# Performance work log

Measured on AMD Instinct MI355X. Metric: run time of the kernel, lower is better.

## Reference

```python
import jax, jax.numpy as jnp
import numpy as np

N = 16384       # pedestrian_num
D_IN = 2        # input_size
H = 64          # hidden_size


def setup_inputs() -> dict:
    key = jax.random.key(0)
    ks = jax.random.split(key, 4)
    data = jax.random.normal(ks[0], (N, D_IN), dtype=jnp.float32)
    # Linear weights stored as [in, out]; scaled like torch default init (~1/sqrt(in)).
    W1 = jax.random.normal(ks[1], (D_IN, 32), dtype=jnp.float32) / np.sqrt(D_IN)
    b1 = jnp.zeros((32,), dtype=jnp.float32)
    W2 = jax.random.normal(ks[2], (32, 64), dtype=jnp.float32) / np.sqrt(32)
    b2 = jnp.zeros((64,), dtype=jnp.float32)
    W3 = jax.random.normal(ks[3], (64, H), dtype=jnp.float32) / np.sqrt(64)
    b3 = jnp.zeros((H,), dtype=jnp.float32)
    return {"data": data, "W1": W1, "b1": b1, "W2": W2, "b2": b2, "W3": W3, "b3": b3}


def reference(data, W1, b1, W2, b2, W3, b3):
    # Per-pedestrian MLP (batched over all N pedestrians at once).
    h = jax.nn.relu(data @ W1 + b1)          # [N, 32]
    h = jax.nn.relu(h @ W2 + b2)             # [N, 64]
    h = h @ W3 + b3                          # [N, H]
    # Spatial affinity: the original fills the lower triangle with <h_i, h_j>
    # and its softmax reads entry [max(i,j), min(i,j)], i.e. the full
    # symmetric Gram matrix G = h @ h.T.
    G = jnp.einsum("nd,md->nm", h, h)        # [N, N], symmetric
    # Row-wise softmax over the symmetric affinity matrix.
    return jax.nn.softmax(G, axis=-1)
```

## Files before the change

kernel.cpp:

```cpp
#include <hip/hip_runtime.h>

#define N     16384
#define DH    64
#define TILE  128
#define NT    (N / TILE)
#define S2    133

typedef __attribute__((ext_vector_type(8))) short  short8;
typedef __attribute__((ext_vector_type(4))) float  f32x4;

__device__ __forceinline__ ushort bf_hi(float x) {
    unsigned u = __float_as_uint(x);
    unsigned r = u + 0x7FFFu + ((u >> 16) & 1u);
    return (ushort)(r >> 16);
}
__device__ __forceinline__ float bf_val(ushort h) {
    return __uint_as_float(((unsigned)h) << 16);
}

__device__ __forceinline__ short8 ldfrag(const ushort* __restrict__ p, int row, int koff) {
    return *(const short8*)(p + (size_t)row * DH + koff);
}

__global__ __launch_bounds__(128) void mlp_kernel(
    const float* __restrict__ data,
    const float* __restrict__ W1, const float* __restrict__ b1,
    const float* __restrict__ W2, const float* __restrict__ b2,
    const float* __restrict__ W3, const float* __restrict__ b3,
    ushort* __restrict__ hHi, ushort* __restrict__ hLo)
{
    __shared__ float sW1[64], sb1[32], sW2[32 * 64], sb2[64], sW3[64 * 64], sb3[64];
    const int tid = threadIdx.x;
    if (tid < 64) sW1[tid] = W1[tid];
    if (tid < 32) sb1[tid] = b1[tid];
    if (tid < 64) sb2[tid] = b2[tid];
    if (tid < 64) sb3[tid] = b3[tid];
    for (int t = tid; t < 32 * 64; t += 128) sW2[t] = W2[t];
    for (int t = tid; t < 64 * 64; t += 128) sW3[t] = W3[t];
    __syncthreads();

    const int i = blockIdx.x * 128 + tid;
    const float x0 = data[2 * i + 0];
    const float x1 = data[2 * i + 1];

    float h1[32];
#pragma unroll
    for (int o = 0; o < 32; ++o)
        h1[o] = fmaxf(0.f, fmaf(x0, sW1[o], fmaf(x1, sW1[32 + o], sb1[o])));

    float h2[64];
#pragma unroll
    for (int o = 0; o < 64; ++o) {
        float a = sb2[o];
#pragma unroll
        for (int k = 0; k < 32; ++k) a = fmaf(h1[k], sW2[k * 64 + o], a);
        h2[o] = fmaxf(0.f, a);
    }

    ushort hs[64], ls[64];
#pragma unroll
    for (int o = 0; o < 64; ++o) {
        float a = sb3[o];
#pragma unroll
        for (int k = 0; k < 64; ++k) a = fmaf(h2[k], sW3[k * 64 + o], a);
        const ushort hb = bf_hi(a);
        hs[o] = hb;
        ls[o] = bf_hi(a - bf_val(hb));
    }
#pragma unroll
    for (int q = 0; q < 8; ++q) {
        short8 vh, vl;
#pragma unroll
        for (int t = 0; t < 8; ++t) { vh[t] = (short)hs[q * 8 + t]; vl[t] = (short)ls[q * 8 + t]; }
        *(short8*)(hHi + (size_t)i * DH + q * 8) = vh;
        *(short8*)(hLo + (size_t)i * DH + q * 8) = vl;
    }
}

__device__ __forceinline__ void stage_B(
    const ushort* __restrict__ hHi, const ushort* __restrict__ hLo,
    int brow0, int tid, ushort* __restrict__ sB)
{
    const int arr = tid >> 7;
    const int r   = tid & 127;
    const ushort* __restrict__ src = (arr ? hLo : hHi) + (size_t)(brow0 + r) * DH;
    ushort* __restrict__ dst = sB + arr * (TILE * DH) + r * 64;
    const int sw = (r & 7);
#pragma unroll
    for (int q = 0; q < 8; ++q) {
        const short8 v = *(const short8*)(src + q * 8);
        *(short8*)(dst + 8 * (q ^ sw)) = v;
    }
}

__device__ __forceinline__ short8 ldB(const ushort* __restrict__ sB,
                                      int arr, int row, int ks, int kb)
{
    return *(const short8*)(sB + arr * (TILE * DH) + row * 64 + 8 * (((ks << 2) + kb) ^ (row & 7)));
}

__device__ __forceinline__ void gram_tile(
    const ushort* __restrict__ hHi, const ushort* __restrict__ hLo,
    const ushort* __restrict__ sB,
    int bi, int wave, int r16, int kb, f32x4 acc[2][8])
{
#pragma unroll
    for (int rb = 0; rb < 2; ++rb)
#pragma unroll
        for (int cb = 0; cb < 8; ++cb) acc[rb][cb] = (f32x4){0.f, 0.f, 0.f, 0.f};

    const int arow = bi * TILE + wave * 16 + r16;
#pragma unroll
    for (int ks = 0; ks < 2; ++ks) {
        const int koff = ks * 32 + kb * 8;
        const short8 Ah0 = ldfrag(hHi, arow,      koff);
        const short8 Ah1 = ldfrag(hHi, arow + 64, koff);
        const short8 Al0 = ldfrag(hLo, arow,      koff);
        const short8 Al1 = ldfrag(hLo, arow + 64, koff);
#pragma unroll
        for (int cb = 0; cb < 8; ++cb) {
            const int brow = cb * 16 + r16;
            const short8 Bh = ldB(sB, 0, brow, ks, kb);
            const short8 Bl = ldB(sB, 1, brow, ks, kb);
            acc[0][cb] = __builtin_amdgcn_mfma_f32_16x16x32_bf16(Ah0, Bh, acc[0][cb], 0, 0, 0);
            acc[0][cb] = __builtin_amdgcn_mfma_f32_16x16x32_bf16(Ah0, Bl, acc[0][cb], 0, 0, 0);
            acc[0][cb] = __builtin_amdgcn_mfma_f32_16x16x32_bf16(Al0, Bh, acc[0][cb], 0, 0, 0);
            acc[1][cb] = __builtin_amdgcn_mfma_f32_16x16x32_bf16(Ah1, Bh, acc[1][cb], 0, 0, 0);
            acc[1][cb] = __builtin_amdgcn_mfma_f32_16x16x32_bf16(Ah1, Bl, acc[1][cb], 0, 0, 0);
            acc[1][cb] = __builtin_amdgcn_mfma_f32_16x16x32_bf16(Al1, Bh, acc[1][cb], 0, 0, 0);
        }
    }
}

__device__ __forceinline__ int tile_row(int wave, int kb, int rb, int reg) {
    return rb * 64 + wave * 16 + kb * 4 + reg;
}

__device__ __forceinline__ void tri_decode(int p, int& bi, int& bj) {
    const int xcd = p & 7, s = p >> 3;
    const int q = s / 129, r = s % 129;
    const int P = xcd * 8 + q;
    if (r <= P) { bi = r;         bj = P;       }
    else        { bi = r - P - 1; bj = 127 - P; }
}

#define SMEM_BYTES 34048

__global__ __launch_bounds__(256, 4) void pass1_mfma(
    const ushort* __restrict__ hHi, const ushort* __restrict__ hLo,
    float* __restrict__ part_m, float* __restrict__ part_l)
{
    int bi, bj;
    tri_decode(blockIdx.x, bi, bj);

    __shared__ __attribute__((aligned(16))) char smem[SMEM_BYTES];
    ushort* sB = (ushort*)smem;
    float*  jm = (float*)smem;
    float*  jl = jm + 512;

    const int tid = threadIdx.x;
    const int wave = tid >> 6, lane = tid & 63;
    const int r16 = lane & 15, kb = lane >> 4;

    stage_B(hHi, hLo, bj * TILE, tid, sB);
    __syncthreads();

    f32x4 acc[2][8];
    gram_tile(hHi, hLo, sB, bi, wave, r16, kb, acc);

#pragma unroll
    for (int rb = 0; rb < 2; ++rb) {
#pragma unroll
        for (int reg = 0; reg < 4; ++reg) {
            float m = acc[rb][0][reg];
#pragma unroll
            for (int cb = 1; cb < 8; ++cb) m = fmaxf(m, acc[rb][cb][reg]);
            m = fmaxf(m, __shfl_xor(m, 1));
            m = fmaxf(m, __shfl_xor(m, 2));
            m = fmaxf(m, __shfl_xor(m, 4));
            m = fmaxf(m, __shfl_xor(m, 8));
            float sum = 0.f;
#pragma unroll
            for (int cb = 0; cb < 8; ++cb) sum += __expf(acc[rb][cb][reg] - m);
            sum += __shfl_xor(sum, 1);
            sum += __shfl_xor(sum, 2);
            sum += __shfl_xor(sum, 4);
            sum += __shfl_xor(sum, 8);
            if (r16 == 0) {
                const int grow = bi * TILE + tile_row(wave, kb, rb, reg);
                part_m[(size_t)bj * N + grow] = m;
                part_l[(size_t)bj * N + grow] = sum;
            }
        }
    }

    if (bi != bj) {
        __syncthreads();
#pragma unroll
        for (int cb = 0; cb < 8; ++cb) {
            float m = acc[0][cb][0];
#pragma unroll
            for (int rb = 0; rb < 2; ++rb)
#pragma unroll
                for (int reg = 0; reg < 4; ++reg) m = fmaxf(m, acc[rb][cb][reg]);
            m = fmaxf(m, __shfl_xor(m, 16));
            m = fmaxf(m, __shfl_xor(m, 32));
            float sum = 0.f;
#pragma unroll
            for (int rb = 0; rb < 2; ++rb)
#pragma unroll
                for (int reg = 0; reg < 4; ++reg) sum += __expf(acc[rb][cb][reg] - m);
            sum += __shfl_xor(sum, 16);
            sum += __shfl_xor(sum, 32);
            if (kb == 0) { jm[wave * 128 + cb * 16 + r16] = m; jl[wave * 128 + cb * 16 + r16] = sum; }
        }
        __syncthreads();
        if (tid < 128) {
            float M = jm[tid];
#pragma unroll
            for (int w = 1; w < 4; ++w) M = fmaxf(M, jm[w * 128 + tid]);
            float L = 0.f;
#pragma unroll
            for (int w = 0; w < 4; ++w) L += jl[w * 128 + tid] * __expf(jm[w * 128 + tid] - M);
            part_m[(size_t)bi * N + bj * TILE + tid] = M;
            part_l[(size_t)bi * N + bj * TILE + tid] = L;
        }
    }
}

__global__ __launch_bounds__(256) void merge_kernel(
    const float* __restrict__ part_m, const float* __restrict__ part_l,
    float* __restrict__ mrow, float* __restrict__ rrow)
{
    const int i = blockIdx.x * 256 + threadIdx.x;
    float M = -3.0e38f;
    for (int o = 0; o < NT; ++o) M = fmaxf(M, part_m[(size_t)o * N + i]);
    float L = 0.f;
    for (int o = 0; o < NT; ++o)
        L = fmaf(part_l[(size_t)o * N + i], __expf(part_m[(size_t)o * N + i] - M), L);
    mrow[i] = M;
    rrow[i] = 1.0f / L;
}

__global__ __launch_bounds__(256, 4) void pass2_mfma(
    const ushort* __restrict__ hHi, const ushort* __restrict__ hLo,
    const float* __restrict__ mrow, const float* __restrict__ rrow,
    float* __restrict__ out)
{
    const int p = blockIdx.x;
    const int xcd = p & 7, slot = p >> 3;
    const int bj = xcd * 16 + (slot & 15);
    const int bi = slot >> 4;

    const int tid = threadIdx.x;
    const int wave = tid >> 6, lane = tid & 63;
    const int r16 = lane & 15, kb = lane >> 4;

    __shared__ __attribute__((aligned(16))) char smem[SMEM_BYTES];
    ushort* sB   = (ushort*)smem;
    float*  ldsP = (float*)smem;

    stage_B(hHi, hLo, bj * TILE, tid, sB);
    __syncthreads();

    f32x4 acc[2][8];
    gram_tile(hHi, hLo, sB, bi, wave, r16, kb, acc);
    __syncthreads();

#pragma unroll
    for (int hh = 0; hh < 2; ++hh) {
#pragma unroll
        for (int reg = 0; reg < 4; ++reg) {
            const int rl   = wave * 16 + kb * 4 + reg;
            const int grow = bi * TILE + hh * 64 + rl;
            const float m  = mrow[grow];
            const float rr = rrow[grow];
#pragma unroll
            for (int cb = 0; cb < 8; ++cb)
                ldsP[rl * S2 + cb * 16 + r16] = __expf(acc[hh][cb][reg] - m) * rr;
        }
        __syncthreads();
#pragma unroll
        for (int qq = 0; qq < 8; ++qq) {
            const int f4 = tid + 256 * qq;
            const int rl = f4 >> 5, c4 = f4 & 31;
            const f32x4 v = *(const f32x4*)&ldsP[rl * S2 + c4 * 4];
            f32x4* dst = (f32x4*)(out + (size_t)(bi * TILE + hh * 64 + rl) * N + bj * TILE + c4 * 4);
            __builtin_nontemporal_store(v, dst);
        }
        __syncthreads();
    }
}

extern "C" void kernel_launch(void* const* d_in, const int* in_sizes, int n_in,
                              void* d_out, int out_size, void* d_ws, size_t ws_size,
                              hipStream_t stream)
{
    const float* data = (const float*)d_in[0];
    const float* W1   = (const float*)d_in[1];
    const float* b1   = (const float*)d_in[2];
    const float* W2   = (const float*)d_in[3];
    const float* b2   = (const float*)d_in[4];
    const float* W3   = (const float*)d_in[5];
    const float* b3   = (const float*)d_in[6];
    float* out = (float*)d_out;

    float* part_m = (float*)d_ws;
    float* part_l = part_m + (size_t)NT * N;
    float* mrow   = part_l + (size_t)NT * N;
    float* rrow   = mrow + N;
    ushort* hHi   = (ushort*)(rrow + N);
    ushort* hLo   = hHi + (size_t)N * DH;

    mlp_kernel<<<N / 128, 128, 0, stream>>>(data, W1, b1, W2, b2, W3, b3, hHi, hLo);
    pass1_mfma<<<NT * (NT + 1) / 2, 256, 0, stream>>>(hHi, hLo, part_m, part_l);
    merge_kernel<<<N / 256, 256, 0, stream>>>(part_m, part_l, mrow, rrow);
    pass2_mfma<<<NT * NT, 256, 0, stream>>>(hHi, hLo, mrow, rrow, out);
}
```

Before: 371.2 us.

## Reshape pass2 tiles to 64x256 for wider row writes and single epilogue

The second softmax pass now computes 64-row by 256-column output tiles instead of 128x128, staging 256 B rows in LDS and using a single LDS transpose/store round. Each output row segment written per block doubles in width, which gives longer contiguous nontemporal stores, and one of the two epilogue barrier phases goes away. The cost is that A-row fragments are reused across fewer rows, the LDS staging footprint grows, and occupancy hints drop to 2 blocks per CU. The block-to-XCD mapping also changes, which affects L2 locality of the B tiles.

```diff
diff --git a/kernel.cpp b/kernel.cpp
--- a/kernel.cpp
+++ b/kernel.cpp
@@ -4,7 +4,10 @@
 #define DH    64
 #define TILE  128
 #define NT    (N / TILE)
-#define S2    133
+
+#define TI    64
+#define TJ    256
+#define S2P   258
 
 typedef __attribute__((ext_vector_type(8))) short  short8;
 typedef __attribute__((ext_vector_type(4))) float  f32x4;
@@ -97,6 +100,31 @@
                                       int arr, int row, int ks, int kb)
 {
     return *(const short8*)(sB + arr * (TILE * DH) + row * 64 + 8 * (((ks << 2) + kb) ^ (row & 7)));
+}
+
+__device__ __forceinline__ void stage_B256(
+    const ushort* __restrict__ hHi, const ushort* __restrict__ hLo,
+    int brow0, int tid, ushort* __restrict__ sB)
+{
+    const int r = tid;
+    const ushort* __restrict__ srcH = hHi + (size_t)(brow0 + r) * DH;
+    const ushort* __restrict__ srcL = hLo + (size_t)(brow0 + r) * DH;
+    ushort* __restrict__ dstH = sB + r * 64;
+    ushort* __restrict__ dstL = sB + (TJ * DH) + r * 64;
+    const int sw = (r & 7);
+#pragma unroll
+    for (int q = 0; q < 8; ++q) {
+        const short8 vh = *(const short8*)(srcH + q * 8);
+        const short8 vl = *(const short8*)(srcL + q * 8);
+        *(short8*)(dstH + 8 * (q ^ sw)) = vh;
+        *(short8*)(dstL + 8 * (q ^ sw)) = vl;
+    }
+}
+
+__device__ __forceinline__ short8 ldB256(const ushort* __restrict__ sB,
+                                         int arr, int row, int ks, int kb)
+{
+    return *(const short8*)(sB + arr * (TJ * DH) + row * 64 + 8 * (((ks << 2) + kb) ^ (row & 7)));
 }
 
 __device__ __forceinline__ void gram_tile(
@@ -144,7 +172,8 @@
     else        { bi = r - P - 1; bj = 127 - P; }
 }
 
-#define SMEM_BYTES 34048
+#define SMEM1_BYTES 32768
+#define SMEM2_BYTES (S2P * TI * 4)
 
 __global__ __launch_bounds__(256, 4) void pass1_mfma(
     const ushort* __restrict__ hHi, const ushort* __restrict__ hLo,
@@ -153,7 +182,7 @@
     int bi, bj;
     tri_decode(blockIdx.x, bi, bj);
 
-    __shared__ __attribute__((aligned(16))) char smem[SMEM_BYTES];
+    __shared__ __attribute__((aligned(16))) char smem[SMEM1_BYTES];
     ushort* sB = (ushort*)smem;
     float*  jm = (float*)smem;
     float*  jl = jm + 512;
@@ -242,53 +271,68 @@
     rrow[i] = 1.0f / L;
 }
 
-__global__ __launch_bounds__(256, 4) void pass2_mfma(
+__global__ __launch_bounds__(256, 2) void pass2_mfma(
     const ushort* __restrict__ hHi, const ushort* __restrict__ hLo,
     const float* __restrict__ mrow, const float* __restrict__ rrow,
     float* __restrict__ out)
 {
     const int p = blockIdx.x;
     const int xcd = p & 7, slot = p >> 3;
-    const int bj = xcd * 16 + (slot & 15);
-    const int bi = slot >> 4;
+    const int bj = xcd * 8 + (slot & 7);
+    const int bi = slot >> 3;
 
     const int tid = threadIdx.x;
     const int wave = tid >> 6, lane = tid & 63;
     const int r16 = lane & 15, kb = lane >> 4;
 
-    __shared__ __attribute__((aligned(16))) char smem[SMEM_BYTES];
+    __shared__ __attribute__((aligned(16))) char smem[SMEM2_BYTES];
     ushort* sB   = (ushort*)smem;
     float*  ldsP = (float*)smem;
 
-    stage_B(hHi, hLo, bj * TILE, tid, sB);
-    __syncthreads();
-
-    f32x4 acc[2][8];
-    gram_tile(hHi, hLo, sB, bi, wave, r16, kb, acc);
-    __syncthreads();
-
-#pragma unroll
-    for (int hh = 0; hh < 2; ++hh) {
-#pragma unroll
-        for (int reg = 0; reg < 4; ++reg) {
-            const int rl   = wave * 16 + kb * 4 + reg;
-            const int grow = bi * TILE + hh * 64 + rl;
-            const float m  = mrow[grow];
-            const float rr = rrow[grow];
-#pragma unroll
-            for (int cb = 0; cb < 8; ++cb)
-                ldsP[rl * S2 + cb * 16 + r16] = __expf(acc[hh][cb][reg] - m) * rr;
-        }
-        __syncthreads();
-#pragma unroll
-        for (int qq = 0; qq < 8; ++qq) {
-            const int f4 = tid + 256 * qq;
-            const int rl = f4 >> 5, c4 = f4 & 31;
-            const f32x4 v = *(const f32x4*)&ldsP[rl * S2 + c4 * 4];
-            f32x4* dst = (f32x4*)(out + (size_t)(bi * TILE + hh * 64 + rl) * N + bj * TILE + c4 * 4);
-            __builtin_nontemporal_store(v, dst);
-        }
-        __syncthreads();
+    stage_B256(hHi, hLo, bj * TJ, tid, sB);
+    __syncthreads();
+
+    f32x4 acc[16];
+#pragma unroll
+    for (int cb = 0; cb < 16; ++cb) acc[cb] = (f32x4){0.f, 0.f, 0.f, 0.f};
+
+    const int arow = bi * TI + wave * 16 + r16;
+#pragma unroll
+    for (int ks = 0; ks < 2; ++ks) {
+        const int koff = ks * 32 + kb * 8;
+        const short8 Ah = ldfrag(hHi, arow, koff);
+        const short8 Al = ldfrag(hLo, arow, koff);
+#pragma unroll
+        for (int cb = 0; cb < 16; ++cb) {
+            const int brow = cb * 16 + r16;
+            const short8 Bh = ldB256(sB, 0, brow, ks, kb);
+            const short8 Bl = ldB256(sB, 1, brow, ks, kb);
+            acc[cb] = __builtin_amdgcn_mfma_f32_16x16x32_bf16(Ah, Bh, acc[cb], 0, 0, 0);
+            acc[cb] = __builtin_amdgcn_mfma_f32_16x16x32_bf16(Ah, Bl, acc[cb], 0, 0, 0);
+            acc[cb] = __builtin_amdgcn_mfma_f32_16x16x32_bf16(Al, Bh, acc[cb], 0, 0, 0);
+        }
+    }
+    __syncthreads();
+
+#pragma unroll
+    for (int reg = 0; reg < 4; ++reg) {
+        const int rl   = wave * 16 + kb * 4 + reg;
+        const int grow = bi * TI + rl;
+        const float m  = mrow[grow];
+        const float rr = rrow[grow];
+#pragma unroll
+        for (int cb = 0; cb < 16; ++cb)
+            ldsP[rl * S2P + cb * 16 + r16] = __expf(acc[cb][reg] - m) * rr;
+    }
+    __syncthreads();
+
+#pragma unroll
+    for (int qq = 0; qq < 16; ++qq) {
+        const int f4 = tid + 256 * qq;
+        const int rl = f4 >> 6, c4 = f4 & 63;
+        const f32x4 v = *(const f32x4*)&ldsP[rl * S2P + c4 * 4];
+        f32x4* dst = (f32x4*)(out + (size_t)(bi * TI + rl) * N + bj * TJ + c4 * 4);
+        __builtin_nontemporal_store(v, dst);
     }
 }
 
@@ -315,5 +359,5 @@
     mlp_kernel<<<N / 128, 128, 0, stream>>>(data, W1, b1, W2, b2, W3, b3, hHi, hLo);
     pass1_mfma<<<NT * (NT + 1) / 2, 256, 0, stream>>>(hHi, hLo, part_m, part_l);
     merge_kernel<<<N / 256, 256, 0, stream>>>(part_m, part_l, mrow, rrow);
-    pass2_mfma<<<NT * NT, 256, 0, stream>>>(hHi, hLo, mrow, rrow, out);
-}
+    pass2_mfma<<<(N / TI) * (N / TJ), 256, 0, stream>>>(hHi, hLo, mrow, rrow, out);
+}
```

Result: slower. 421.0 us (+13.4%).

## Make pass2 persistent over 16 row tiles and fold normalizer into log-sum-exp

Applied to the files above, without the earlier changes.

Each pass2 block now stages its B column tile once and loops over 16 row tiles, cutting the grid from 16384 to 1024 blocks and reusing the staged B data. The merge kernel emits a single log-sum-exp value per row, so pass2 computes exp(g - s) without a separate multiply and reads one array instead of two. LDS for B and the P staging buffer are now separate, and the occupancy hint drops to 2 blocks per CU, which may reduce latency hiding for the write-bound output stage.

```diff
diff --git a/kernel.cpp b/kernel.cpp
--- a/kernel.cpp
+++ b/kernel.cpp
@@ -144,7 +144,7 @@
     else        { bi = r - P - 1; bj = 127 - P; }
 }
 
-#define SMEM_BYTES 34048
+#define SMEM1_BYTES 32768
 
 __global__ __launch_bounds__(256, 4) void pass1_mfma(
     const ushort* __restrict__ hHi, const ushort* __restrict__ hLo,
@@ -153,7 +153,7 @@
     int bi, bj;
     tri_decode(blockIdx.x, bi, bj);
 
-    __shared__ __attribute__((aligned(16))) char smem[SMEM_BYTES];
+    __shared__ __attribute__((aligned(16))) char smem[SMEM1_BYTES];
     ushort* sB = (ushort*)smem;
     float*  jm = (float*)smem;
     float*  jl = jm + 512;
@@ -230,7 +230,7 @@
 
 __global__ __launch_bounds__(256) void merge_kernel(
     const float* __restrict__ part_m, const float* __restrict__ part_l,
-    float* __restrict__ mrow, float* __restrict__ rrow)
+    float* __restrict__ srow)
 {
     const int i = blockIdx.x * 256 + threadIdx.x;
     float M = -3.0e38f;
@@ -238,57 +238,57 @@
     float L = 0.f;
     for (int o = 0; o < NT; ++o)
         L = fmaf(part_l[(size_t)o * N + i], __expf(part_m[(size_t)o * N + i] - M), L);
-    mrow[i] = M;
-    rrow[i] = 1.0f / L;
-}
-
-__global__ __launch_bounds__(256, 4) void pass2_mfma(
+    srow[i] = M + __logf(L);
+}
+
+__global__ __launch_bounds__(256, 2) void pass2_mfma(
     const ushort* __restrict__ hHi, const ushort* __restrict__ hLo,
-    const float* __restrict__ mrow, const float* __restrict__ rrow,
+    const float* __restrict__ srow,
     float* __restrict__ out)
 {
     const int p = blockIdx.x;
     const int xcd = p & 7, slot = p >> 3;
-    const int bj = xcd * 16 + (slot & 15);
-    const int bi = slot >> 4;
+    const int bj  = xcd * 16 + (slot & 15);
+    const int bi0 = (slot >> 4) * 16;
 
     const int tid = threadIdx.x;
     const int wave = tid >> 6, lane = tid & 63;
     const int r16 = lane & 15, kb = lane >> 4;
 
-    __shared__ __attribute__((aligned(16))) char smem[SMEM_BYTES];
-    ushort* sB   = (ushort*)smem;
-    float*  ldsP = (float*)smem;
+    __shared__ __attribute__((aligned(16))) ushort sB[2 * TILE * DH];
+    __shared__ float ldsP[64 * S2];
 
     stage_B(hHi, hLo, bj * TILE, tid, sB);
     __syncthreads();
 
-    f32x4 acc[2][8];
-    gram_tile(hHi, hLo, sB, bi, wave, r16, kb, acc);
-    __syncthreads();
-
-#pragma unroll
-    for (int hh = 0; hh < 2; ++hh) {
-#pragma unroll
-        for (int reg = 0; reg < 4; ++reg) {
-            const int rl   = wave * 16 + kb * 4 + reg;
-            const int grow = bi * TILE + hh * 64 + rl;
-            const float m  = mrow[grow];
-            const float rr = rrow[grow];
-#pragma unroll
-            for (int cb = 0; cb < 8; ++cb)
-                ldsP[rl * S2 + cb * 16 + r16] = __expf(acc[hh][cb][reg] - m) * rr;
-        }
-        __syncthreads();
-#pragma unroll
-        for (int qq = 0; qq < 8; ++qq) {
-            const int f4 = tid + 256 * qq;
-            const int rl = f4 >> 5, c4 = f4 & 31;
-            const f32x4 v = *(const f32x4*)&ldsP[rl * S2 + c4 * 4];
-            f32x4* dst = (f32x4*)(out + (size_t)(bi * TILE + hh * 64 + rl) * N + bj * TILE + c4 * 4);
-            __builtin_nontemporal_store(v, dst);
-        }
-        __syncthreads();
+    for (int it = 0; it < 16; ++it) {
+        const int bi = bi0 + it;
+
+        f32x4 acc[2][8];
+        gram_tile(hHi, hLo, sB, bi, wave, r16, kb, acc);
+
+#pragma unroll
+        for (int hh = 0; hh < 2; ++hh) {
+#pragma unroll
+            for (int reg = 0; reg < 4; ++reg) {
+                const int rl   = wave * 16 + kb * 4 + reg;
+                const int grow = bi * TILE + hh * 64 + rl;
+                const float s  = srow[grow];
+#pragma unroll
+                for (int cb = 0; cb < 8; ++cb)
+                    ldsP[rl * S2 + cb * 16 + r16] = __expf(acc[hh][cb][reg] - s);
+            }
+            __syncthreads();
+#pragma unroll
+            for (int qq = 0; qq < 8; ++qq) {
+                const int f4 = tid + 256 * qq;
+                const int rl = f4 >> 5, c4 = f4 & 31;
+                const f32x4 v = *(const f32x4*)&ldsP[rl * S2 + c4 * 4];
+                f32x4* dst = (f32x4*)(out + (size_t)(bi * TILE + hh * 64 + rl) * N + bj * TILE + c4 * 4);
+                __builtin_nontemporal_store(v, dst);
+            }
+            __syncthreads();
+        }
     }
 }
 
@@ -307,13 +307,12 @@
 
     float* part_m = (float*)d_ws;
     float* part_l = part_m + (size_t)NT * N;
-    float* mrow   = part_l + (size_t)NT * N;
-    float* rrow   = mrow + N;
-    ushort* hHi   = (ushort*)(rrow + N);
+    float* srow   = part_l + (size_t)NT * N;
+    ushort* hHi   = (ushort*)(srow + 2 * N);
     ushort* hLo   = hHi + (size_t)N * DH;
 
     mlp_kernel<<<N / 128, 128, 0, stream>>>(data, W1, b1, W2, b2, W3, b3, hHi, hLo);
     pass1_mfma<<<NT * (NT + 1) / 2, 256, 0, stream>>>(hHi, hLo, part_m, part_l);
-    merge_kernel<<<N / 256, 256, 0, stream>>>(part_m, part_l, mrow, rrow);
-    pass2_mfma<<<NT * NT, 256, 0, stream>>>(hHi, hLo, mrow, rrow, out);
-}
+    merge_kernel<<<N / 256, 256, 0, stream>>>(part_m, part_l, srow);
+    pass2_mfma<<<1024, 256, 0, stream>>>(hHi, hLo, srow, out);
+}
```

Measured after the change: 355.8 us. -4.1%, faster.
